# Performance work log

Hardware: AMD Instinct MI355X
Metric: run time of the kernel (lower is better)

## Reference

```python
import jax, jax.numpy as jnp
import numpy as np

N = 500_000
D = 256
H = 10
G = 8192


def setup_inputs() -> dict:
    key = jax.random.key(0)
    k1, k2, k3 = jax.random.split(key, 3)
    features = jax.random.normal(k1, (N, D), dtype=jnp.float32)
    W = jax.random.normal(k2, (D, H), dtype=jnp.float32) * 0.0625  # ~1/sqrt(256)
    b = jnp.zeros((H,), dtype=jnp.float32)
    segment_ids = jnp.sort(jax.random.randint(k3, (N,), 0, G, dtype=jnp.int32))
    return {"features": features, "W": W, "b": b,
            "segment_ids": segment_ids, "num_segments": G}


def reference(features, W, b, segment_ids, num_segments):
    # weights: sigmoid(Linear(256 -> 10)) applied per node
    weights = jax.nn.sigmoid(features @ W + b)            # [N, H]
    # denominator: per-graph sum of weights -> [G, H]
    denom = jax.ops.segment_sum(weights, segment_ids, num_segments=num_segments)
    # numerator: per-graph sum of f[n] (outer) w[n]; loop over the H=10 heads
    # to avoid materializing an [N, H, D] intermediate.
    num = jnp.stack(
        [jax.ops.segment_sum(features * weights[:, k:k + 1], segment_ids,
                             num_segments=num_segments)
         for k in range(weights.shape[1])],
        axis=1)                                           # [G, H, D]
    keys = num / denom[:, :, None]                        # weighted mean
    return keys
```

## Files before the change

### kernel.cpp

```cpp
#include <hip/hip_runtime.h>
#include <hip/hip_bf16.h>
#include <math.h>

#define HH 10
#define DD 256

template<int CTRL>
__device__ __forceinline__ float dpp_add(float v) {
  int t = __builtin_amdgcn_mov_dpp(__float_as_int(v), CTRL, 0xF, 0xF, true);
  return v + __int_as_float(t);
}

__device__ __forceinline__ float wave_sum64(float v) {
  v = dpp_add<0xB1>(v);
  v = dpp_add<0x4E>(v);
  v = dpp_add<0x141>(v);
  v = dpp_add<0x140>(v);
  v += __shfl_xor(v, 16, 64);
  v += __shfl_xor(v, 32, 64);
  return v;
}

__global__ void seg_offsets_kernel(const int* __restrict__ seg, int n, int G,
                                   int* __restrict__ off) {
  int i = blockIdx.x * blockDim.x + threadIdx.x;
  if (i >= n) return;
  int cur = seg[i];
  int prev = (i == 0) ? -1 : seg[i - 1];
  for (int g = prev + 1; g <= cur; ++g) off[g] = i;
  if (i == n - 1) {
    for (int g = cur + 1; g <= G; ++g) off[g] = n;
  }
}

__global__ __launch_bounds__(256) void seg_pool_kernel(
    const float* __restrict__ feat, const float* __restrict__ W,
    const float* __restrict__ b, const int* __restrict__ off,
    float* __restrict__ out, int G) {
  const int lane = threadIdx.x & 63;
  const int g = blockIdx.x * 4 + (threadIdx.x >> 6);
  if (g >= G) return;

  float wreg[4][HH];
  {
    const float* wp = W + lane * 4 * HH;
#pragma unroll
    for (int j = 0; j < 4; ++j)
#pragma unroll
      for (int k = 0; k < HH; ++k) wreg[j][k] = wp[j * HH + k];
  }
  float bias[HH];
#pragma unroll
  for (int k = 0; k < HH; ++k) bias[k] = b[k];

  float acc[HH][4];
  float dsum[HH];
#pragma unroll
  for (int k = 0; k < HH; ++k) {
    dsum[k] = 0.f;
    acc[k][0] = acc[k][1] = acc[k][2] = acc[k][3] = 0.f;
  }

  const int s = off[g];
  const int e = off[g + 1];

  if (s < e) {
    const float* fp = feat + (size_t)s * DD + lane * 4;
    float4 f = *reinterpret_cast<const float4*>(fp);

    for (int n = s; n < e; ++n) {
      float4 fn;
      if (n + 1 < e)
        fn = *reinterpret_cast<const float4*>(fp + (size_t)(n + 1 - s) * DD);

      float p[HH];
#pragma unroll
      for (int k = 0; k < HH; ++k) {
        float t = f.x * wreg[0][k];
        t = fmaf(f.y, wreg[1][k], t);
        t = fmaf(f.z, wreg[2][k], t);
        t = fmaf(f.w, wreg[3][k], t);
        p[k] = t;
      }
#pragma unroll
      for (int k = 0; k < HH; ++k) p[k] = wave_sum64(p[k]);

#pragma unroll
      for (int k = 0; k < HH; ++k) {
        float x = p[k] + bias[k];
        float wgt = __builtin_amdgcn_rcpf(1.f + __expf(-x));
        dsum[k] += wgt;
        acc[k][0] = fmaf(wgt, f.x, acc[k][0]);
        acc[k][1] = fmaf(wgt, f.y, acc[k][1]);
        acc[k][2] = fmaf(wgt, f.z, acc[k][2]);
        acc[k][3] = fmaf(wgt, f.w, acc[k][3]);
      }

      f = fn;
    }
  }

  float* op = out + ((size_t)g * HH) * DD + lane * 4;
#pragma unroll
  for (int k = 0; k < HH; ++k) {
    float r = __builtin_amdgcn_rcpf(dsum[k]);
    float4 o = make_float4(acc[k][0] * r, acc[k][1] * r,
                           acc[k][2] * r, acc[k][3] * r);
    *reinterpret_cast<float4*>(op + (size_t)k * DD) = o;
  }
}

extern "C" void kernel_launch(void* const* d_in, const int* in_sizes, int n_in,
                              void* d_out, int out_size, void* d_ws, size_t ws_size,
                              hipStream_t stream) {
  const float* feat = (const float*)d_in[0];
  const float* W    = (const float*)d_in[1];
  const float* b    = (const float*)d_in[2];
  const int*   seg  = (const int*)d_in[3];
  float* out = (float*)d_out;

  const int H_ = in_sizes[2];
  const int D_ = in_sizes[1] / H_;
  const int N  = in_sizes[0] / D_;
  const int G  = out_size / (H_ * D_);

  int* off = (int*)d_ws;

  seg_offsets_kernel<<<(N + 255) / 256, 256, 0, stream>>>(seg, N, G, off);
  seg_pool_kernel<<<(G + 3) / 4, 256, 0, stream>>>(feat, W, b, off, out, G);
}
```

Baseline: 767.1 us.

## Split each segment across four waves with LDS reduction and deeper prefetch

Instead of one wave per segment, each block now handles one segment and its four waves process interleaved rows. The waves' partial accumulators and denominators are combined through shared memory, and wave 0 writes the normalized output. The loop also prefetches two rows ahead, using clamped indices for the tail. This raises parallelism per segment and hides memory latency better, at the cost of an LDS reduction, a block barrier, and redundant clamped loads at the tail.

```diff
diff --git a/kernel.cpp b/kernel.cpp
--- a/kernel.cpp
+++ b/kernel.cpp
@@ -4,6 +4,7 @@
 
 #define HH 10
 #define DD 256
+#define WPS 4
 
 template<int CTRL>
 __device__ __forceinline__ float dpp_add(float v) {
@@ -36,10 +37,13 @@
 __global__ __launch_bounds__(256) void seg_pool_kernel(
     const float* __restrict__ feat, const float* __restrict__ W,
     const float* __restrict__ b, const int* __restrict__ off,
-    float* __restrict__ out, int G) {
+    float* __restrict__ out) {
   const int lane = threadIdx.x & 63;
-  const int g = blockIdx.x * 4 + (threadIdx.x >> 6);
-  if (g >= G) return;
+  const int wv = threadIdx.x >> 6;
+  const int g = blockIdx.x;
+
+  __shared__ float lacc[WPS - 1][64][HH * 4];
+  __shared__ float ldsum[WPS][HH];
 
   float wreg[4][HH];
   {
@@ -63,23 +67,30 @@
 
   const int s = off[g];
   const int e = off[g + 1];
+  const int m = e - s;
+  const int cnt = (m > wv) ? ((m - wv + WPS - 1) >> 2) : 0;
 
-  if (s < e) {
-    const float* fp = feat + (size_t)s * DD + lane * 4;
-    float4 f = *reinterpret_cast<const float4*>(fp);
+  if (cnt > 0) {
+    const int last = e - 1;
+    auto rowp = [&](int i) {
+      int idx = s + wv + (i << 2);
+      if (idx > last) idx = last;
+      return reinterpret_cast<const float4*>(feat + (size_t)idx * DD + lane * 4);
+    };
 
-    for (int n = s; n < e; ++n) {
-      float4 fn;
-      if (n + 1 < e)
-        fn = *reinterpret_cast<const float4*>(fp + (size_t)(n + 1 - s) * DD);
+    float4 f0 = *rowp(0);
+    float4 f1 = *rowp(1);
+
+    for (int i = 0; i < cnt; ++i) {
+      float4 fn = *rowp(i + 2);
 
       float p[HH];
 #pragma unroll
       for (int k = 0; k < HH; ++k) {
-        float t = f.x * wreg[0][k];
-        t = fmaf(f.y, wreg[1][k], t);
-        t = fmaf(f.z, wreg[2][k], t);
-        t = fmaf(f.w, wreg[3][k], t);
+        float t = f0.x * wreg[0][k];
+        t = fmaf(f0.y, wreg[1][k], t);
+        t = fmaf(f0.z, wreg[2][k], t);
+        t = fmaf(f0.w, wreg[3][k], t);
         p[k] = t;
       }
 #pragma unroll
@@ -90,23 +101,46 @@
         float x = p[k] + bias[k];
         float wgt = __builtin_amdgcn_rcpf(1.f + __expf(-x));
         dsum[k] += wgt;
-        acc[k][0] = fmaf(wgt, f.x, acc[k][0]);
-        acc[k][1] = fmaf(wgt, f.y, acc[k][1]);
-        acc[k][2] = fmaf(wgt, f.z, acc[k][2]);
-        acc[k][3] = fmaf(wgt, f.w, acc[k][3]);
+        acc[k][0] = fmaf(wgt, f0.x, acc[k][0]);
+        acc[k][1] = fmaf(wgt, f0.y, acc[k][1]);
+        acc[k][2] = fmaf(wgt, f0.z, acc[k][2]);
+        acc[k][3] = fmaf(wgt, f0.w, acc[k][3]);
       }
 
-      f = fn;
+      f0 = f1;
+      f1 = fn;
     }
   }
 
-  float* op = out + ((size_t)g * HH) * DD + lane * 4;
+  if (wv > 0) {
+    float* lp = &lacc[wv - 1][lane][0];
 #pragma unroll
-  for (int k = 0; k < HH; ++k) {
-    float r = __builtin_amdgcn_rcpf(dsum[k]);
-    float4 o = make_float4(acc[k][0] * r, acc[k][1] * r,
-                           acc[k][2] * r, acc[k][3] * r);
-    *reinterpret_cast<float4*>(op + (size_t)k * DD) = o;
+    for (int k = 0; k < HH; ++k) {
+      float4 v4 = make_float4(acc[k][0], acc[k][1], acc[k][2], acc[k][3]);
+      *reinterpret_cast<float4*>(lp + k * 4) = v4;
+    }
+  }
+  if (lane == 0) {
+#pragma unroll
+    for (int k = 0; k < HH; ++k) ldsum[wv][k] = dsum[k];
+  }
+  __syncthreads();
+
+  if (wv == 0) {
+    float* op = out + ((size_t)g * HH) * DD + lane * 4;
+#pragma unroll
+    for (int k = 0; k < HH; ++k) {
+      float4 a = make_float4(acc[k][0], acc[k][1], acc[k][2], acc[k][3]);
+#pragma unroll
+      for (int w = 0; w < WPS - 1; ++w) {
+        float4 t = *reinterpret_cast<const float4*>(&lacc[w][lane][k * 4]);
+        a.x += t.x; a.y += t.y; a.z += t.z; a.w += t.w;
+      }
+      float ds = ldsum[0][k] + ldsum[1][k] + ldsum[2][k] + ldsum[3][k];
+      float r = __builtin_amdgcn_rcpf(ds);
+      float4 o = make_float4(a.x * r, a.y * r, a.z * r, a.w * r);
+      *reinterpret_cast<float4*>(op + (size_t)k * DD) = o;
+    }
   }
 }
 
@@ -127,5 +161,5 @@
   int* off = (int*)d_ws;
 
   seg_offsets_kernel<<<(N + 255) / 256, 256, 0, stream>>>(seg, N, G, off);
-  seg_pool_kernel<<<(G + 3) / 4, 256, 0, stream>>>(feat, W, b, off, out, G);
+  seg_pool_kernel<<<G, 256, 0, stream>>>(feat, W, b, off, out);
 }
```

After: 748.3 us. 1.03x faster.

## Compute per-row sigmoid weights lane-per-row in chunks, broadcast via readlane

Applied to the files above, without the earlier changes.

Each wave now takes chunks of 64 rows. Each lane computes the full 256-wide dot products for one row, reading W as uniform scalar loads, which removes the per-row 10x wave-wide DPP/shuffle reductions. The weights are then broadcast to the wave with readlane during a second pass that accumulates the weighted features. In exchange, every feature row is read twice, and the first pass has each lane reading a whole row on its own (strided, uncoalesced), which puts more pressure on cache and memory.

```diff
diff --git a/kernel.cpp b/kernel.cpp
--- a/kernel.cpp
+++ b/kernel.cpp
@@ -4,22 +4,8 @@
 
 #define HH 10
 #define DD 256
-
-template<int CTRL>
-__device__ __forceinline__ float dpp_add(float v) {
-  int t = __builtin_amdgcn_mov_dpp(__float_as_int(v), CTRL, 0xF, 0xF, true);
-  return v + __int_as_float(t);
-}
-
-__device__ __forceinline__ float wave_sum64(float v) {
-  v = dpp_add<0xB1>(v);
-  v = dpp_add<0x4E>(v);
-  v = dpp_add<0x141>(v);
-  v = dpp_add<0x140>(v);
-  v += __shfl_xor(v, 16, 64);
-  v += __shfl_xor(v, 32, 64);
-  return v;
-}
+#define SPB 4
+#define CHUNK 64
 
 __global__ void seg_offsets_kernel(const int* __restrict__ seg, int n, int G,
                                    int* __restrict__ off) {
@@ -33,25 +19,17 @@
   }
 }
 
+__device__ __forceinline__ float readlane_f(float v, int srclane) {
+  return __int_as_float(__builtin_amdgcn_readlane(__float_as_int(v), srclane));
+}
+
 __global__ __launch_bounds__(256) void seg_pool_kernel(
     const float* __restrict__ feat, const float* __restrict__ W,
     const float* __restrict__ b, const int* __restrict__ off,
     float* __restrict__ out, int G) {
   const int lane = threadIdx.x & 63;
-  const int g = blockIdx.x * 4 + (threadIdx.x >> 6);
+  const int g = blockIdx.x * SPB + (threadIdx.x >> 6);
   if (g >= G) return;
-
-  float wreg[4][HH];
-  {
-    const float* wp = W + lane * 4 * HH;
-#pragma unroll
-    for (int j = 0; j < 4; ++j)
-#pragma unroll
-      for (int k = 0; k < HH; ++k) wreg[j][k] = wp[j * HH + k];
-  }
-  float bias[HH];
-#pragma unroll
-  for (int k = 0; k < HH; ++k) bias[k] = b[k];
 
   float acc[HH][4];
   float dsum[HH];
@@ -64,39 +42,48 @@
   const int s = off[g];
   const int e = off[g + 1];
 
-  if (s < e) {
-    const float* fp = feat + (size_t)s * DD + lane * 4;
-    float4 f = *reinterpret_cast<const float4*>(fp);
+  for (int base = s; base < e; base += CHUNK) {
+    const int mc = min(CHUNK, e - base);
 
-    for (int n = s; n < e; ++n) {
-      float4 fn;
-      if (n + 1 < e)
-        fn = *reinterpret_cast<const float4*>(fp + (size_t)(n + 1 - s) * DD);
+    const int myrow = base + ((lane < mc) ? lane : (mc - 1));
+    const float* fr = feat + (size_t)myrow * DD;
 
-      float p[HH];
+    float x[HH];
+#pragma unroll
+    for (int k = 0; k < HH; ++k) x[k] = 0.f;
+
+    for (int d4 = 0; d4 < DD / 4; ++d4) {
+      const float4 f = *reinterpret_cast<const float4*>(fr + d4 * 4);
+      const float* wp = W + (size_t)d4 * 4 * HH;
 #pragma unroll
       for (int k = 0; k < HH; ++k) {
-        float t = f.x * wreg[0][k];
-        t = fmaf(f.y, wreg[1][k], t);
-        t = fmaf(f.z, wreg[2][k], t);
-        t = fmaf(f.w, wreg[3][k], t);
-        p[k] = t;
+        float t = fmaf(f.x, wp[0 * HH + k], x[k]);
+        t = fmaf(f.y, wp[1 * HH + k], t);
+        t = fmaf(f.z, wp[2 * HH + k], t);
+        t = fmaf(f.w, wp[3 * HH + k], t);
+        x[k] = t;
       }
+    }
+
+    float w[HH];
 #pragma unroll
-      for (int k = 0; k < HH; ++k) p[k] = wave_sum64(p[k]);
+    for (int k = 0; k < HH; ++k) {
+      float xx = x[k] + b[k];
+      w[k] = __builtin_amdgcn_rcpf(1.f + __expf(-xx));
+    }
 
+    const float* fp2 = feat + (size_t)base * DD + lane * 4;
+    for (int n = 0; n < mc; ++n) {
+      const float4 f = *reinterpret_cast<const float4*>(fp2 + (size_t)n * DD);
 #pragma unroll
       for (int k = 0; k < HH; ++k) {
-        float x = p[k] + bias[k];
-        float wgt = __builtin_amdgcn_rcpf(1.f + __expf(-x));
-        dsum[k] += wgt;
-        acc[k][0] = fmaf(wgt, f.x, acc[k][0]);
-        acc[k][1] = fmaf(wgt, f.y, acc[k][1]);
-        acc[k][2] = fmaf(wgt, f.z, acc[k][2]);
-        acc[k][3] = fmaf(wgt, f.w, acc[k][3]);
+        const float wk = readlane_f(w[k], n);
+        dsum[k] += wk;
+        acc[k][0] = fmaf(wk, f.x, acc[k][0]);
+        acc[k][1] = fmaf(wk, f.y, acc[k][1]);
+        acc[k][2] = fmaf(wk, f.z, acc[k][2]);
+        acc[k][3] = fmaf(wk, f.w, acc[k][3]);
       }
-
-      f = fn;
     }
   }
 
@@ -127,5 +114,6 @@
   int* off = (int*)d_ws;
 
   seg_offsets_kernel<<<(N + 255) / 256, 256, 0, stream>>>(seg, N, G, off);
-  seg_pool_kernel<<<(G + 3) / 4, 256, 0, stream>>>(feat, W, b, off, out, G);
+  seg_pool_kernel<<<(G + SPB - 1) / SPB, 256, 0, stream>>>(feat, W, b, off,
+                                                           out, G);
 }
```

Result: slower. 820.4 us (+6.9%).
